# Kernel tuning notes

Hardware: AMD Instinct MI355X
Metric: run time of the kernel (lower is better)

The kernel has to match this reference:

```python
import jax, jax.numpy as jnp
import numpy as np
import math

SCALE = 16
R_MAX = 4
ALPHA_DYN = 2.0


def _bilinear_down(x, Ho, Wo):
    # torch F.interpolate bilinear, align_corners=False, no antialias. x: [C,H,W]
    C, H, W = x.shape
    def coords(no, ni):
        src = jnp.maximum((jnp.arange(no, dtype=jnp.float32) + 0.5) * (ni / no) - 0.5, 0.0)
        i0 = jnp.floor(src).astype(jnp.int32)
        t = src - i0.astype(jnp.float32)
        return jnp.clip(i0, 0, ni - 1), jnp.clip(i0 + 1, 0, ni - 1), t
    r0, r1, tr = coords(Ho, H)
    c0, c1, tc = coords(Wo, W)
    x = x[:, r0, :] * (1.0 - tr)[None, :, None] + x[:, r1, :] * tr[None, :, None]
    x = x[:, :, c0] * (1.0 - tc)[None, None, :] + x[:, :, c1] * tc[None, None, :]
    return x


def _jbu(feat_lr, guide_hr, sx_raw, sy_raw, th_raw, sr_raw):
    B, C, Hl, Wl = feat_lr.shape
    Hh, Wh = guide_hr.shape[2], guide_hr.shape[3]

    # parameter transforms
    up = lambda p: jnp.repeat(jnp.repeat(p[0, 0], SCALE, axis=0), SCALE, axis=1)  # nearest, exact multiple
    sx = jnp.maximum(up(jnp.exp(sx_raw)), 1e-6)
    sy = jnp.maximum(up(jnp.exp(sy_raw)), 1e-6)
    th = up(math.pi * jnp.tanh(th_raw))
    sr = jnp.maximum(up(jnp.exp(sr_raw)), 1e-6)

    Yh, Xh = jnp.meshgrid(jnp.arange(Hh, dtype=jnp.float32), jnp.arange(Wh, dtype=jnp.float32), indexing='ij')
    uc = jnp.round((Yh + 0.5) / SCALE - 0.5).astype(jnp.int32)
    vc = jnp.round((Xh + 0.5) / SCALE - 0.5).astype(jnp.int32)

    R_map_sq = jnp.clip(ALPHA_DYN * jnp.maximum(sx, sy), 1.0, float(R_MAX)) ** 2
    guide_lr = _bilinear_down(guide_hr[0], Hl, Wl)  # [Cg,Hl,Wl]
    cos_t, sin_t = jnp.cos(th), jnp.sin(th)
    inv2sx2 = 1.0 / (2.0 * sx ** 2 + 1e-8)
    inv2sy2 = 1.0 / (2.0 * sy ** 2 + 1e-8)
    inv2sr2 = 1.0 / (2.0 * sr ** 2 + 1e-8)

    d = jnp.arange(-R_MAX, R_MAX + 1, dtype=jnp.int32)
    dys, dxs = jnp.meshgrid(d, d, indexing='ij')
    offs = jnp.stack([dys.ravel(), dxs.ravel()], axis=1)  # [(2R+1)^2, 2]

    g_hr = guide_hr[0]    # [Cg,Hh,Wh]
    f_lr = feat_lr[0]     # [C,Hl,Wl]

    def step(carry, off):
        num, den = carry
        dy, dx = off[0], off[1]
        ui = jnp.clip(uc + dy, 0, Hl - 1)  # [Hh,Wh] int32
        vi = jnp.clip(vc + dx, 0, Wl - 1)
        cur_dx = (Xh - (vi.astype(jnp.float32) * SCALE + (SCALE - 1) / 2.0)) / SCALE
        cur_dy = (Yh - (ui.astype(jnp.float32) * SCALE + (SCALE - 1) / 2.0)) / SCALE
        a = cur_dx * cos_t + cur_dy * sin_t
        b = -cur_dx * sin_t + cur_dy * cos_t
        g_lr_s = guide_lr[:, ui, vi]                       # [Cg,Hh,Wh] gather
        g_diff2 = jnp.sum((g_hr - g_lr_s) ** 2, axis=0)    # [Hh,Wh]
        log_w = -(a ** 2) * inv2sx2 - (b ** 2) * inv2sy2 - g_diff2 * inv2sr2
        mask = (dy * dy + dx * dx).astype(jnp.float32) <= R_map_sq
        w = jnp.exp(log_w) * mask.astype(jnp.float32)      # [Hh,Wh]
        f_s = f_lr[:, ui, vi]                              # [C,Hh,Wh] gather
        return (num + f_s * w[None], den + w), None

    num0 = jnp.zeros((C, Hh, Wh), jnp.float32)
    den0 = jnp.zeros((Hh, Wh), jnp.float32)
    (num, den), _ = jax.lax.scan(step, (num0, den0), offs)
    res = num / jnp.maximum(den, 1e-8)
    return res[None].astype(feat_lr.dtype)


def setup_inputs() -> dict:
    key = jax.random.key(0)
    k1, k2 = jax.random.split(key)
    feat_lr = jax.random.normal(k1, (1, 128, 32, 32), jnp.float32)
    guide_hr = jax.random.normal(k2, (1, 3, 512, 512), jnp.float32)
    sx_raw = jnp.full((1, 1, 32, 32), float(np.log(16.0)), jnp.float32)
    sy_raw = jnp.full((1, 1, 32, 32), float(np.log(16.0)), jnp.float32)
    th_raw = jnp.zeros((1, 1, 32, 32), jnp.float32)
    sr_raw = jnp.full((1, 1, 32, 32), float(np.log(0.12)), jnp.float32)
    return {"feat_lr": feat_lr, "guide_hr": guide_hr, "sx_raw": sx_raw,
            "sy_raw": sy_raw, "th_raw": th_raw, "sr_raw": sr_raw}


def reference(feat_lr, guide_hr, sx_raw, sy_raw, th_raw, sr_raw):
    return _jbu(feat_lr, guide_hr, sx_raw, sy_raw, th_raw, sr_raw)
```

## Files before the change

### kernel.cpp

```cpp
#include <hip/hip_runtime.h>
#include <math.h>

#define HH 512
#define WH 512
#define L2E 1.44269504f
#define PI_F 3.14159265358979323846f
#define FTK 104

typedef __attribute__((ext_vector_type(8))) short short8v;
typedef __attribute__((ext_vector_type(4))) float float4v;


__global__ __launch_bounds__(256) void prep_kernel(
    const float* __restrict__ feat,
    const float* __restrict__ guide,
    float* __restrict__ ws)
{
    const int gid = blockIdx.x * 256 + threadIdx.x;
    float* glr = ws;
    unsigned short* featT = (unsigned short*)(ws + 4096);
    if (gid < 131072) {
        const int cell = gid >> 7;
        const int c    = gid & 127;
        const float v  = feat[c * 1024 + cell];
        const unsigned int b = __float_as_uint(v);
        featT[gid] = (unsigned short)((b + 0x7FFFu + ((b >> 16) & 1u)) >> 16);
    }
    if (gid < 1024) {
        const int u = gid >> 5, v = gid & 31;
        const int y0 = u * 16 + 7, x0 = v * 16 + 7;
        #pragma unroll
        for (int ch = 0; ch < 3; ++ch) {
            const float* g = guide + ch * (HH * WH);
            const float s = g[y0 * WH + x0] + g[y0 * WH + x0 + 1]
                          + g[(y0 + 1) * WH + x0] + g[(y0 + 1) * WH + x0 + 1];
            glr[gid * 4 + ch] = 0.25f * s;
        }
        glr[gid * 4 + 3] = 0.0f;
    }
}

__global__ __launch_bounds__(512, 1) void jbu_kernel(
    const float* __restrict__ guide,
    const float* __restrict__ sx_raw,
    const float* __restrict__ sy_raw,
    const float* __restrict__ th_raw,
    const float* __restrict__ sr_raw,
    const float* __restrict__ ws,
    float* __restrict__ out)
{
    __shared__ __align__(16) unsigned short FT[2 * 128 * FTK];
    __shared__ float tabK[192], tabA[192], tabB[192], tabG0[192], tabG1[192], tabG2[192];
    __shared__ float hdr[2][6];

    const float* glr = ws;
    const unsigned short* featT = (const unsigned short*)(ws + 4096);

    const int tid = threadIdx.x;
    const int u = blockIdx.x >> 4;
    const int v = (blockIdx.x & 15) << 1;

    if (tid < 192) {
        const int c2 = tid / 96;
        const int k  = tid - c2 * 96;
        const int cu = u, cv = v + c2;
        const int cell = cu * 32 + cv;
        const float sx = fmaxf(__expf(sx_raw[cell]), 1e-6f);
        const float sy = fmaxf(__expf(sy_raw[cell]), 1e-6f);
        const float thv = PI_F * tanhf(th_raw[cell]);
        const float sr = fmaxf(__expf(sr_raw[cell]), 1e-6f);
        const float R  = fminf(fmaxf(2.0f * fmaxf(sx, sy), 1.0f), 4.0f);
        const float cth = cosf(thv), sth = sinf(thv);
        const float i2sx = 1.0f / (2.0f * sx * sx + 1e-8f);
        const float i2sy = 1.0f / (2.0f * sy * sy + 1e-8f);
        const float i2sr = 1.0f / (2.0f * sr * sr + 1e-8f);
        if (k == 0) {
            hdr[c2][0] = cth; hdr[c2][1] = sth;
            hdr[c2][2] = i2sx * L2E; hdr[c2][3] = i2sy * L2E; hdr[c2][4] = i2sr * L2E;
        }
        const int k9 = k / 9;
        const int dy = k9 - 4, dx = k - k9 * 9 - 4;
        const int act = (k < 81) && ((float)(dy * dy + dx * dx) <= R * R);
        const int ui = min(max(cu + dy, 0), 31);
        const int vi = min(max(cv + dx, 0), 31);
        const float rk = (float)(vi - cv), tk = (float)(ui - cu);
        const float ak = rk * cth + tk * sth;
        const float bk = tk * cth - rk * sth;
        const float gl0 = glr[(ui * 32 + vi) * 4 + 0];
        const float gl1 = glr[(ui * 32 + vi) * 4 + 1];
        const float gl2 = glr[(ui * 32 + vi) * 4 + 2];
        tabK[tid]  = act ? -(ak * ak * i2sx + bk * bk * i2sy
                             + (gl0 * gl0 + gl1 * gl1 + gl2 * gl2) * i2sr) * L2E
                         : -1e30f;
        tabA[tid]  = 2.0f * ak * i2sx * L2E;
        tabB[tid]  = 2.0f * bk * i2sy * L2E;
        tabG0[tid] = 2.0f * gl0 * i2sr * L2E;
        tabG1[tid] = 2.0f * gl1 * i2sr * L2E;
        tabG2[tid] = 2.0f * gl2 * i2sr * L2E;
    }

    for (int s = tid; s < 3072; s += 512) {
        const int k   = s % 96;
        const int cg  = (s / 96) & 15;
        const int c2s = s / 1536;
        unsigned short vals[8] = {0, 0, 0, 0, 0, 0, 0, 0};
        if (k < 81) {
            const int k9 = k / 9;
            const int dy = k9 - 4, dx = k - k9 * 9 - 4;
            const int ui = min(max(u + dy, 0), 31);
            const int vi = min(max(v + c2s + dx, 0), 31);
            *(uint4*)vals = *(const uint4*)(featT + (ui * 32 + vi) * 128 + cg * 8);
        }
        const int chb = c2s * 128 + cg * 8;
        #pragma unroll
        for (int j = 0; j < 8; ++j)
            FT[(chb + j) * FTK + k] = vals[j];
    }
    __syncthreads();

    const int wave = tid >> 6;
    const int lane = tid & 63;
    const int lg   = lane >> 4;
    const int pxx  = lane & 15;
    const int c2   = wave >> 2;
    const int mtb  = (wave & 3) * 4;
    const int cv   = v + c2;

    const float cth = hdr[c2][0], sth = hdr[c2][1];
    const float i2sxl = hdr[c2][2], i2syl = hdr[c2][3], i2srl = hdr[c2][4];
    const float qd = ((float)pxx - 7.5f) * 0.0625f;

    float a0[4], b0[4], P[4], g0[4], g1[4], g2[4];
    #pragma unroll
    for (int mt = 0; mt < 4; ++mt) {
        const int y = u * 16 + mtb + mt;
        const int o = y * WH + cv * 16 + pxx;
        g0[mt] = guide[o];
        g1[mt] = guide[HH * WH + o];
        g2[mt] = guide[2 * HH * WH + o];
        const float pd = ((float)(mtb + mt) - 7.5f) * 0.0625f;
        a0[mt] = qd * cth + pd * sth;
        b0[mt] = pd * cth - qd * sth;
        P[mt] = -(a0[mt] * a0[mt] * i2sxl + b0[mt] * b0[mt] * i2syl
                  + (g0[mt] * g0[mt] + g1[mt] * g1[mt] + g2[mt] * g2[mt]) * i2srl);
    }

    short8v Afrag[4][3];
    float den[4] = {0.f, 0.f, 0.f, 0.f};
    const int tb = c2 * 96;
    #pragma unroll
    for (int ks = 0; ks < 3; ++ks) {
        float cK[8], cA[8], cB[8], cG0[8], cG1[8], cG2[8];
        #pragma unroll
        for (int i = 0; i < 8; ++i) {
            const int k = tb + ks * 32 + lg * 8 + i;
            cK[i] = tabK[k];  cA[i] = tabA[k];  cB[i] = tabB[k];
            cG0[i] = tabG0[k]; cG1[i] = tabG1[k]; cG2[i] = tabG2[k];
        }
        #pragma unroll
        for (int mt = 0; mt < 4; ++mt) {
            short8v av;
            #pragma unroll
            for (int i = 0; i < 8; ++i) {
                float lw = P[mt] + cK[i];
                lw = fmaf(a0[mt], cA[i], lw);
                lw = fmaf(b0[mt], cB[i], lw);
                lw = fmaf(g0[mt], cG0[i], lw);
                lw = fmaf(g1[mt], cG1[i], lw);
                lw = fmaf(g2[mt], cG2[i], lw);
                const float w = __builtin_amdgcn_exp2f(lw);
                den[mt] += w;
                const unsigned int b = __float_as_uint(w);
                av[i] = (short)((b + 0x7FFFu + ((b >> 16) & 1u)) >> 16);
            }
            Afrag[mt][ks] = av;
        }
    }

    float invd[4][4];
    #pragma unroll
    for (int mt = 0; mt < 4; ++mt) {
        float d = den[mt];
        d += __shfl_xor(d, 16);
        d += __shfl_xor(d, 32);
        const float id = 1.0f / fmaxf(d, 1e-8f);
        #pragma unroll
        for (int r = 0; r < 4; ++r)
            invd[mt][r] = __shfl(id, lg * 4 + r);
    }

    #pragma unroll
    for (int q = 0; q < 2; ++q) {
        short8v Bf[4][3];
        #pragma unroll
        for (int nt = 0; nt < 4; ++nt) {
            #pragma unroll
            for (int ks = 0; ks < 3; ++ks) {
                const int ch = q * 64 + nt * 16 + pxx;
                Bf[nt][ks] = *(const short8v*)&FT[(c2 * 128 + ch) * FTK + ks * 32 + lg * 8];
            }
        }
        #pragma unroll
        for (int mt = 0; mt < 4; ++mt) {
            float4v acc[4] = {{0.f,0.f,0.f,0.f}, {0.f,0.f,0.f,0.f},
                              {0.f,0.f,0.f,0.f}, {0.f,0.f,0.f,0.f}};
            #pragma unroll
            for (int nt = 0; nt < 4; ++nt)
                #pragma unroll
                for (int ks = 0; ks < 3; ++ks)
                    acc[nt] = __builtin_amdgcn_mfma_f32_16x16x32_bf16(
                        Afrag[mt][ks], Bf[nt][ks], acc[nt], 0, 0, 0);
            const int y = u * 16 + mtb + mt;
            const size_t pix = (size_t)(y * WH + cv * 16 + lg * 4);
            #pragma unroll
            for (int nt = 0; nt < 4; ++nt) {
                const int ch = q * 64 + nt * 16 + pxx;
                float4v res;
                res[0] = acc[nt][0] * invd[mt][0];
                res[1] = acc[nt][1] * invd[mt][1];
                res[2] = acc[nt][2] * invd[mt][2];
                res[3] = acc[nt][3] * invd[mt][3];
                *(float4v*)(out + (size_t)ch * (HH * WH) + pix) = res;
            }
        }
    }
}

extern "C" void kernel_launch(void* const* d_in, const int* in_sizes, int n_in,
                              void* d_out, int out_size, void* d_ws, size_t ws_size,
                              hipStream_t stream) {
    const float* feat   = (const float*)d_in[0];
    const float* guide  = (const float*)d_in[1];
    const float* sx_raw = (const float*)d_in[2];
    const float* sy_raw = (const float*)d_in[3];
    const float* th_raw = (const float*)d_in[4];
    const float* sr_raw = (const float*)d_in[5];
    float* out = (float*)d_out;
    float* ws  = (float*)d_ws;

    prep_kernel<<<512, 256, 0, stream>>>(feat, guide, ws);
    jbu_kernel<<<512, 512, 0, stream>>>(guide, sx_raw, sy_raw, th_raw, sr_raw, ws, out);
}
```

Measured before the change: 42.58 us.

## Fuse prep into JBU kernel with one cell per block and nontemporal stores

Removes the separate prep kernel and its workspace round trip. Each block now gathers its feature neighbourhood directly from fp32 input, converts it to bf16 in shared memory, and computes the low-res guide averages inline. Blocks shrink to 256 threads handling a single cell, with a swizzled block order and a launch-bounds occupancy hint of three blocks. Output is written with nontemporal stores. This saves one launch and the dependency between kernels, at the cost of redundant scalar gathers of the feature map (about 81x128 per block) and redundant guide reads.

```diff
diff --git a/kernel.cpp b/kernel.cpp
--- a/kernel.cpp
+++ b/kernel.cpp
@@ -10,111 +10,78 @@
 typedef __attribute__((ext_vector_type(8))) short short8v;
 typedef __attribute__((ext_vector_type(4))) float float4v;
 
-
-__global__ __launch_bounds__(256) void prep_kernel(
+__global__ __launch_bounds__(256, 3) void jbu_fused_kernel(
     const float* __restrict__ feat,
-    const float* __restrict__ guide,
-    float* __restrict__ ws)
-{
-    const int gid = blockIdx.x * 256 + threadIdx.x;
-    float* glr = ws;
-    unsigned short* featT = (unsigned short*)(ws + 4096);
-    if (gid < 131072) {
-        const int cell = gid >> 7;
-        const int c    = gid & 127;
-        const float v  = feat[c * 1024 + cell];
-        const unsigned int b = __float_as_uint(v);
-        featT[gid] = (unsigned short)((b + 0x7FFFu + ((b >> 16) & 1u)) >> 16);
-    }
-    if (gid < 1024) {
-        const int u = gid >> 5, v = gid & 31;
-        const int y0 = u * 16 + 7, x0 = v * 16 + 7;
-        #pragma unroll
-        for (int ch = 0; ch < 3; ++ch) {
-            const float* g = guide + ch * (HH * WH);
-            const float s = g[y0 * WH + x0] + g[y0 * WH + x0 + 1]
-                          + g[(y0 + 1) * WH + x0] + g[(y0 + 1) * WH + x0 + 1];
-            glr[gid * 4 + ch] = 0.25f * s;
-        }
-        glr[gid * 4 + 3] = 0.0f;
-    }
-}
-
-__global__ __launch_bounds__(512, 1) void jbu_kernel(
     const float* __restrict__ guide,
     const float* __restrict__ sx_raw,
     const float* __restrict__ sy_raw,
     const float* __restrict__ th_raw,
     const float* __restrict__ sr_raw,
-    const float* __restrict__ ws,
     float* __restrict__ out)
 {
-    __shared__ __align__(16) unsigned short FT[2 * 128 * FTK];
-    __shared__ float tabK[192], tabA[192], tabB[192], tabG0[192], tabG1[192], tabG2[192];
-    __shared__ float hdr[2][6];
+    __shared__ __align__(16) unsigned short FT[128 * FTK];
+    __shared__ float tabK[96], tabA[96], tabB[96];
+    __shared__ float tabG0[96], tabG1[96], tabG2[96];
+    __shared__ float hdr[6];
 
-    const float* glr = ws;
-    const unsigned short* featT = (const unsigned short*)(ws + 4096);
+    const int tid  = threadIdx.x;
+    const int cell = (blockIdx.x & 7) * 128 + (blockIdx.x >> 3);
+    const int cu = cell >> 5, cv = cell & 31;
 
-    const int tid = threadIdx.x;
-    const int u = blockIdx.x >> 4;
-    const int v = (blockIdx.x & 15) << 1;
-
-    if (tid < 192) {
-        const int c2 = tid / 96;
-        const int k  = tid - c2 * 96;
-        const int cu = u, cv = v + c2;
-        const int cell = cu * 32 + cv;
-        const float sx = fmaxf(__expf(sx_raw[cell]), 1e-6f);
-        const float sy = fmaxf(__expf(sy_raw[cell]), 1e-6f);
+    if (tid < 96) {
+        const int k = tid;
+        const float sx  = fmaxf(__expf(sx_raw[cell]), 1e-6f);
+        const float sy  = fmaxf(__expf(sy_raw[cell]), 1e-6f);
         const float thv = PI_F * tanhf(th_raw[cell]);
-        const float sr = fmaxf(__expf(sr_raw[cell]), 1e-6f);
-        const float R  = fminf(fmaxf(2.0f * fmaxf(sx, sy), 1.0f), 4.0f);
+        const float sr  = fmaxf(__expf(sr_raw[cell]), 1e-6f);
+        const float R   = fminf(fmaxf(2.0f * fmaxf(sx, sy), 1.0f), 4.0f);
         const float cth = cosf(thv), sth = sinf(thv);
         const float i2sx = 1.0f / (2.0f * sx * sx + 1e-8f);
         const float i2sy = 1.0f / (2.0f * sy * sy + 1e-8f);
         const float i2sr = 1.0f / (2.0f * sr * sr + 1e-8f);
         if (k == 0) {
-            hdr[c2][0] = cth; hdr[c2][1] = sth;
-            hdr[c2][2] = i2sx * L2E; hdr[c2][3] = i2sy * L2E; hdr[c2][4] = i2sr * L2E;
+            hdr[0] = cth; hdr[1] = sth;
+            hdr[2] = i2sx * L2E; hdr[3] = i2sy * L2E; hdr[4] = i2sr * L2E;
         }
         const int k9 = k / 9;
         const int dy = k9 - 4, dx = k - k9 * 9 - 4;
         const int act = (k < 81) && ((float)(dy * dy + dx * dx) <= R * R);
         const int ui = min(max(cu + dy, 0), 31);
         const int vi = min(max(cv + dx, 0), 31);
+        const int y0 = ui * 16 + 7, x0 = vi * 16 + 7;
+        float gl[3];
+        #pragma unroll
+        for (int ch = 0; ch < 3; ++ch) {
+            const float* g = guide + ch * (HH * WH);
+            gl[ch] = 0.25f * (g[y0 * WH + x0] + g[y0 * WH + x0 + 1]
+                            + g[(y0 + 1) * WH + x0] + g[(y0 + 1) * WH + x0 + 1]);
+        }
         const float rk = (float)(vi - cv), tk = (float)(ui - cu);
         const float ak = rk * cth + tk * sth;
         const float bk = tk * cth - rk * sth;
-        const float gl0 = glr[(ui * 32 + vi) * 4 + 0];
-        const float gl1 = glr[(ui * 32 + vi) * 4 + 1];
-        const float gl2 = glr[(ui * 32 + vi) * 4 + 2];
-        tabK[tid]  = act ? -(ak * ak * i2sx + bk * bk * i2sy
-                             + (gl0 * gl0 + gl1 * gl1 + gl2 * gl2) * i2sr) * L2E
-                         : -1e30f;
-        tabA[tid]  = 2.0f * ak * i2sx * L2E;
-        tabB[tid]  = 2.0f * bk * i2sy * L2E;
-        tabG0[tid] = 2.0f * gl0 * i2sr * L2E;
-        tabG1[tid] = 2.0f * gl1 * i2sr * L2E;
-        tabG2[tid] = 2.0f * gl2 * i2sr * L2E;
+        tabK[k]  = act ? -(ak * ak * i2sx + bk * bk * i2sy
+                           + (gl[0]*gl[0] + gl[1]*gl[1] + gl[2]*gl[2]) * i2sr) * L2E
+                       : -1e30f;
+        tabA[k]  = 2.0f * ak * i2sx * L2E;
+        tabB[k]  = 2.0f * bk * i2sy * L2E;
+        tabG0[k] = 2.0f * gl[0] * i2sr * L2E;
+        tabG1[k] = 2.0f * gl[1] * i2sr * L2E;
+        tabG2[k] = 2.0f * gl[2] * i2sr * L2E;
     }
 
-    for (int s = tid; s < 3072; s += 512) {
-        const int k   = s % 96;
-        const int cg  = (s / 96) & 15;
-        const int c2s = s / 1536;
-        unsigned short vals[8] = {0, 0, 0, 0, 0, 0, 0, 0};
+    for (int it = 0; it < 48; ++it) {
+        const int s  = tid + it * 256;
+        const int ch = s / 96;
+        const int k  = s - ch * 96;
+        float fv = 0.f;
         if (k < 81) {
             const int k9 = k / 9;
-            const int dy = k9 - 4, dx = k - k9 * 9 - 4;
-            const int ui = min(max(u + dy, 0), 31);
-            const int vi = min(max(v + c2s + dx, 0), 31);
-            *(uint4*)vals = *(const uint4*)(featT + (ui * 32 + vi) * 128 + cg * 8);
+            const int ui = min(max(cu + k9 - 4, 0), 31);
+            const int vi = min(max(cv + (k - k9 * 9) - 4, 0), 31);
+            fv = feat[ch * 1024 + ui * 32 + vi];
         }
-        const int chb = c2s * 128 + cg * 8;
-        #pragma unroll
-        for (int j = 0; j < 8; ++j)
-            FT[(chb + j) * FTK + k] = vals[j];
+        const unsigned int b = __float_as_uint(fv);
+        FT[ch * FTK + k] = (unsigned short)((b + 0x7FFFu + ((b >> 16) & 1u)) >> 16);
     }
     __syncthreads();
 
@@ -122,18 +89,16 @@
     const int lane = tid & 63;
     const int lg   = lane >> 4;
     const int pxx  = lane & 15;
-    const int c2   = wave >> 2;
-    const int mtb  = (wave & 3) * 4;
-    const int cv   = v + c2;
+    const int mtb  = wave * 4;
 
-    const float cth = hdr[c2][0], sth = hdr[c2][1];
-    const float i2sxl = hdr[c2][2], i2syl = hdr[c2][3], i2srl = hdr[c2][4];
+    const float cth = hdr[0], sth = hdr[1];
+    const float i2sxl = hdr[2], i2syl = hdr[3], i2srl = hdr[4];
     const float qd = ((float)pxx - 7.5f) * 0.0625f;
 
     float a0[4], b0[4], P[4], g0[4], g1[4], g2[4];
     #pragma unroll
     for (int mt = 0; mt < 4; ++mt) {
-        const int y = u * 16 + mtb + mt;
+        const int y = cu * 16 + mtb + mt;
         const int o = y * WH + cv * 16 + pxx;
         g0[mt] = guide[o];
         g1[mt] = guide[HH * WH + o];
@@ -141,19 +106,18 @@
         const float pd = ((float)(mtb + mt) - 7.5f) * 0.0625f;
         a0[mt] = qd * cth + pd * sth;
         b0[mt] = pd * cth - qd * sth;
-        P[mt] = -(a0[mt] * a0[mt] * i2sxl + b0[mt] * b0[mt] * i2syl
-                  + (g0[mt] * g0[mt] + g1[mt] * g1[mt] + g2[mt] * g2[mt]) * i2srl);
+        P[mt]  = -(a0[mt]*a0[mt]*i2sxl + b0[mt]*b0[mt]*i2syl
+                   + (g0[mt]*g0[mt] + g1[mt]*g1[mt] + g2[mt]*g2[mt]) * i2srl);
     }
 
     short8v Afrag[4][3];
     float den[4] = {0.f, 0.f, 0.f, 0.f};
-    const int tb = c2 * 96;
     #pragma unroll
     for (int ks = 0; ks < 3; ++ks) {
         float cK[8], cA[8], cB[8], cG0[8], cG1[8], cG2[8];
         #pragma unroll
         for (int i = 0; i < 8; ++i) {
-            const int k = tb + ks * 32 + lg * 8 + i;
+            const int k = ks * 32 + lg * 8 + i;
             cK[i] = tabK[k];  cA[i] = tabA[k];  cB[i] = tabB[k];
             cG0[i] = tabG0[k]; cG1[i] = tabG1[k]; cG2[i] = tabG2[k];
         }
@@ -190,38 +154,27 @@
     }
 
     #pragma unroll
-    for (int q = 0; q < 2; ++q) {
-        short8v Bf[4][3];
+    for (int nt = 0; nt < 8; ++nt) {
+        const int ch = nt * 16 + pxx;
+        short8v Bf[3];
         #pragma unroll
-        for (int nt = 0; nt < 4; ++nt) {
-            #pragma unroll
-            for (int ks = 0; ks < 3; ++ks) {
-                const int ch = q * 64 + nt * 16 + pxx;
-                Bf[nt][ks] = *(const short8v*)&FT[(c2 * 128 + ch) * FTK + ks * 32 + lg * 8];
-            }
-        }
+        for (int ks = 0; ks < 3; ++ks)
+            Bf[ks] = *(const short8v*)&FT[ch * FTK + ks * 32 + lg * 8];
         #pragma unroll
         for (int mt = 0; mt < 4; ++mt) {
-            float4v acc[4] = {{0.f,0.f,0.f,0.f}, {0.f,0.f,0.f,0.f},
-                              {0.f,0.f,0.f,0.f}, {0.f,0.f,0.f,0.f}};
+            float4v acc = {0.f, 0.f, 0.f, 0.f};
             #pragma unroll
-            for (int nt = 0; nt < 4; ++nt)
-                #pragma unroll
-                for (int ks = 0; ks < 3; ++ks)
-                    acc[nt] = __builtin_amdgcn_mfma_f32_16x16x32_bf16(
-                        Afrag[mt][ks], Bf[nt][ks], acc[nt], 0, 0, 0);
-            const int y = u * 16 + mtb + mt;
-            const size_t pix = (size_t)(y * WH + cv * 16 + lg * 4);
-            #pragma unroll
-            for (int nt = 0; nt < 4; ++nt) {
-                const int ch = q * 64 + nt * 16 + pxx;
-                float4v res;
-                res[0] = acc[nt][0] * invd[mt][0];
-                res[1] = acc[nt][1] * invd[mt][1];
-                res[2] = acc[nt][2] * invd[mt][2];
-                res[3] = acc[nt][3] * invd[mt][3];
-                *(float4v*)(out + (size_t)ch * (HH * WH) + pix) = res;
-            }
+            for (int ks = 0; ks < 3; ++ks)
+                acc = __builtin_amdgcn_mfma_f32_16x16x32_bf16(
+                    Afrag[mt][ks], Bf[ks], acc, 0, 0, 0);
+            const int y = cu * 16 + mtb + mt;
+            float4v res;
+            res[0] = acc[0] * invd[mt][0];
+            res[1] = acc[1] * invd[mt][1];
+            res[2] = acc[2] * invd[mt][2];
+            res[3] = acc[3] * invd[mt][3];
+            __builtin_nontemporal_store(
+                res, (float4v*)(out + (size_t)ch * (HH * WH) + y * WH + cv * 16 + lg * 4));
         }
     }
 }
@@ -236,8 +189,8 @@
     const float* th_raw = (const float*)d_in[4];
     const float* sr_raw = (const float*)d_in[5];
     float* out = (float*)d_out;
-    float* ws  = (float*)d_ws;
+    (void)d_ws; (void)ws_size;
 
-    prep_kernel<<<512, 256, 0, stream>>>(feat, guide, ws);
-    jbu_kernel<<<512, 512, 0, stream>>>(guide, sx_raw, sy_raw, th_raw, sr_raw, ws, out);
+    jbu_fused_kernel<<<1024, 256, 0, stream>>>(feat, guide, sx_raw, sy_raw,
+                                               th_raw, sr_raw, out);
 }
```

Measured after the change: 61.72 us. 1.45x slower.
